# Performance work log

Measured on AMD Instinct MI355X. Metric: run time of the kernel, lower is better.

The kernel has to match this reference:

```python
import jax, jax.numpy as jnp
import numpy as np

EPS = 1e-10
BETA = 1.0  # beta passed to VectorQuantizer in Encoder_conv


def _conv(x, w, b, stride, pad):
    # x: NCHW, w: OIHW
    y = jax.lax.conv_general_dilated(x, w, window_strides=stride, padding=pad,
                                     dimension_numbers=('NCHW', 'OIHW', 'NCHW'))
    if b is not None:
        y = y + b[None, :, None, None]
    return y


def _forward(x, w_in, b_in, w_h1, b_h1, w_h2, b_h2, w_h3, b_h3,
             r0_w1, r0_w2, r1_w1, r1_w2, emb):
    relu = jax.nn.relu
    h = relu(_conv(x, w_in, b_in, (2, 2), [(1, 1), (1, 1)]))      # [B,128,256,256]
    h = relu(_conv(h, w_h1, b_h1, (4, 4), [(2, 2), (2, 2)]))      # [B,256,64,64]
    h = relu(_conv(h, w_h2, b_h2, (4, 4), [(2, 2), (2, 2)]))      # [B,256,16,16]
    h = relu(_conv(h, w_h3, b_h3, (2, 2), [(1, 1), (1, 1)]))      # [B,256,8,8]
    # ResidualBlock with 2 Residual layers: relu->conv[1,3]->relu->conv[1,1], no bias
    for wa, wb in ((r0_w1, r0_w2), (r1_w1, r1_w2)):
        t = _conv(relu(h), wa, None, (1, 1), [(0, 0), (1, 1)])
        t = _conv(relu(t), wb, None, (1, 1), [(0, 0), (0, 0)])
        h = h + t
    h = relu(h)
    # VectorQuantizer
    lat = jnp.transpose(h, (0, 2, 3, 1))                          # [B,H,W,D]
    D = emb.shape[1]
    flat = lat.reshape(-1, D)                                     # [N,D]
    dist = (jnp.sum(flat * flat, axis=1, keepdims=True)
            + jnp.sum(emb * emb, axis=1)
            - 2.0 * flat @ emb.T)                                 # [N,K]
    idx = jnp.argmin(dist, axis=1)                                # [N]
    quant = emb[idx].reshape(lat.shape)                           # [B,H,W,D]
    sg = jax.lax.stop_gradient
    e_loss = jnp.mean((sg(quant) - lat) ** 2)
    q_loss = jnp.mean((quant - sg(lat)) ** 2)
    loss = q_loss + BETA * e_loss
    quant_st = lat + sg(quant - lat)                              # straight-through
    probs = jnp.mean(jax.nn.one_hot(idx, emb.shape[0], dtype=lat.dtype), axis=0)
    perplexity = jnp.exp(-jnp.sum(probs * jnp.log(probs + EPS)))
    return jnp.transpose(quant_st, (0, 3, 1, 2)), loss, perplexity


def setup_inputs() -> dict:
    key = jax.random.key(0)
    ks = jax.random.split(key, 14)
    C_in, C, K = 3, 256, 512
    s = 0.05
    f32 = jnp.float32
    return {
        'x':     jax.random.normal(ks[0], (8, C_in, 512, 512), f32),
        'w_in':  jax.random.normal(ks[1], (C // 2, C_in, 4, 4), f32) * s,
        'b_in':  jnp.zeros((C // 2,), f32),
        'w_h1':  jax.random.normal(ks[2], (C, C // 2, 7, 7), f32) * s,
        'b_h1':  jnp.zeros((C,), f32),
        'w_h2':  jax.random.normal(ks[3], (C, C, 7, 7), f32) * s,
        'b_h2':  jnp.zeros((C,), f32),
        'w_h3':  jax.random.normal(ks[4], (C, C, 3, 3), f32) * s,
        'b_h3':  jnp.zeros((C,), f32),
        'r0_w1': jax.random.normal(ks[5], (4 * C, C, 1, 3), f32) * s,
        'r0_w2': jax.random.normal(ks[6], (C, 4 * C, 1, 1), f32) * s,
        'r1_w1': jax.random.normal(ks[7], (4 * C, C, 1, 3), f32) * s,
        'r1_w2': jax.random.normal(ks[8], (C, 4 * C, 1, 1), f32) * s,
        'emb':   jax.random.uniform(ks[9], (K, C), f32, -1.0 / K, 1.0 / K),
    }


def reference(x, w_in, b_in, w_h1, b_h1, w_h2, b_h2, w_h3, b_h3,
              r0_w1, r0_w2, r1_w1, r1_w2, emb):
    return _forward(x, w_in, b_in, w_h1, b_h1, w_h2, b_h2, w_h3, b_h3,
                    r0_w1, r0_w2, r1_w1, r1_w2, emb)
```

## Files before the change

### kernel.cpp

```cpp
#include <hip/hip_runtime.h>
#include <hip/hip_bf16.h>

typedef __hip_bfloat16 bf16;
typedef __attribute__((ext_vector_type(4))) float f32x4;
typedef __attribute__((ext_vector_type(8))) short short8;

__device__ __forceinline__ float b2f(bf16 v) { return __bfloat162float(v); }
__device__ __forceinline__ ushort f2bu(float v)
{
    bf16 b = __float2bfloat16(v);
    return *(ushort*)&b;
}
__device__ __forceinline__ uint relu2(uint v)
{
    uint r = v;
    if (r & 0x8000u)     r &= 0xFFFF0000u;
    if (r & 0x80000000u) r &= 0x0000FFFFu;
    return r;
}
__device__ __forceinline__ uint packbf2(float a, float b)
{
    uint lo = f2bu(a), hi = f2bu(b);
    return lo | (hi << 16);
}

typedef const __attribute__((address_space(1))) unsigned int* as1_u32;
typedef __attribute__((address_space(3))) unsigned int* as3_u32;
__device__ __forceinline__ void gld16(const void* g, uint* l)
{
    __builtin_amdgcn_global_load_lds((as1_u32)g, (as3_u32)l, 16, 0, 0);
}

__global__ void init_k(const float* __restrict__ w_in, const float* __restrict__ w_h1,
        const float* __restrict__ w_h2, const float* __restrict__ w_h3,
        const float* __restrict__ r0w1, const float* __restrict__ r0w2,
        const float* __restrict__ r1w1, const float* __restrict__ r1w2,
        const float* __restrict__ emb,
        bf16* __restrict__ wp1, bf16* __restrict__ wpack2, bf16* __restrict__ wpack3,
        bf16* __restrict__ wp4, bf16* __restrict__ wpA0, bf16* __restrict__ wpA1,
        bf16* __restrict__ wpB0, bf16* __restrict__ wpB1,
        float* __restrict__ en, float* __restrict__ mse, int* __restrict__ hist,
        float* __restrict__ zpad)
{
    long long i = (long long)blockIdx.x * 256 + threadIdx.x;
    if (i < 8192) {
        int j = i & 7; int co = (i >> 3) & 127; int kb = i >> 10;
        int k = kb * 8 + j;
        wp1[i] = __float2bfloat16(k < 48 ? w_in[co * 48 + k] : 0.f);
        return;
    }
    i -= 8192;
    if (i < 1638400) {
        int cil = i & 7; int co = (i >> 3) & 255; int r = i >> 11;
        int cib8 = r % 16; int tap = r / 16;
        float v = (tap < 49) ? w_h1[(size_t)co * 6272 + (cib8 * 8 + cil) * 49 + tap] : 0.f;
        wpack2[i] = __float2bfloat16(v);
        return;
    }
    i -= 1638400;
    if (i < 3276800) {
        int cil = i & 7; int co = (i >> 3) & 255; int r = i >> 11;
        int cib8 = r % 32; int tap = r / 32;
        float v = (tap < 49) ? w_h2[(size_t)co * 12544 + (cib8 * 8 + cil) * 49 + tap] : 0.f;
        wpack3[i] = __float2bfloat16(v);
        return;
    }
    i -= 3276800;
    if (i < 589824) {
        int cil = i & 7; int co = (i >> 3) & 255; int r = i >> 11;
        int cib8 = r % 32; int tap = r / 32;
        wp4[i] = __float2bfloat16(w_h3[(size_t)co * 2304 + (cib8 * 8 + cil) * 9 + tap]);
        return;
    }
    i -= 589824;
    if (i < 786432) {
        int cil = i & 7; int co = (i >> 3) & 1023; int r = i >> 13;
        int cib8 = r % 32; int tap = r / 32;
        wpA0[i] = __float2bfloat16(r0w1[(size_t)co * 768 + (cib8 * 8 + cil) * 3 + tap]);
        return;
    }
    i -= 786432;
    if (i < 786432) {
        int cil = i & 7; int co = (i >> 3) & 1023; int r = i >> 13;
        int cib8 = r % 32; int tap = r / 32;
        wpA1[i] = __float2bfloat16(r1w1[(size_t)co * 768 + (cib8 * 8 + cil) * 3 + tap]);
        return;
    }
    i -= 786432;
    if (i < 262144) {
        int cil = i & 7; int co = (i >> 3) & 255; int cib8 = (i >> 11) % 128;
        wpB0[i] = __float2bfloat16(r0w2[(size_t)co * 1024 + cib8 * 8 + cil]);
        return;
    }
    i -= 262144;
    if (i < 262144) {
        int cil = i & 7; int co = (i >> 3) & 255; int cib8 = (i >> 11) % 128;
        wpB1[i] = __float2bfloat16(r1w2[(size_t)co * 1024 + cib8 * 8 + cil]);
        return;
    }
    i -= 262144;
    if (i < 512) {
        const float* e = emb + (size_t)i * 256;
        float s = 0.f;
        for (int d = 0; d < 256; ++d) { float v = e[d]; s += v * v; }
        en[i] = s;
        return;
    }
    i -= 512;
    if (i < 577) {
        if (i == 0) mse[0] = 0.f;
        else if (i < 513) hist[i - 1] = 0;
        else zpad[i - 513] = 0.f;
    }
}

__global__ __launch_bounds__(256) void conv1m_k(const float* __restrict__ x,
        const bf16* __restrict__ wp1, const float* __restrict__ bias,
        bf16* __restrict__ h1c)
{
    int bid = blockIdx.x;
    int pxt = bid & 511, img = bid >> 9;
    int tr = pxt >> 4, tc = pxt & 15;
    int oh0 = tr * 8, ow0 = tc * 16;
    const float* xi = x + (size_t)img * 786432;
    bf16* oT = h1c + (size_t)img * 8388608;

    int t = threadIdx.x;
    int wave = t >> 6, lane = t & 63;
    int quad = lane >> 4, l15 = lane & 15;

    __shared__ ushort xs[4 * 640];
    __shared__ ushort ot[128 * 136];

    int ihb = oh0 * 2 - 1, iwb = ow0 * 2 - 1;
    for (int i = t; i < 1836; i += 256) {
        int ci = i / 612; int r1 = i - ci * 612;
        int ihl = r1 / 34, iwl = r1 - ihl * 34;
        int ih = ihb + ihl, iw = iwb + iwl;
        float v = 0.f;
        if ((unsigned)ih < 512u && (unsigned)iw < 512u)
            v = xi[ci * 262144 + ih * 512 + iw];
        xs[ci * 640 + ihl * 35 + iwl] = f2bu(v);
    }
    for (int i = t; i < 640; i += 256) xs[3 * 640 + i] = 0;
    __syncthreads();

    f32x4 zero = {0.f, 0.f, 0.f, 0.f};
    f32x4 acc[8][2];
    #pragma unroll
    for (int m = 0; m < 8; ++m) { acc[m][0] = zero; acc[m][1] = zero; }

    int ci_b = quad >> 1;
    int kh0 = (quad & 1) * 2;
    int iwl0 = 2 * l15;

    #pragma unroll
    for (int ks = 0; ks < 2; ++ks) {
        union { short8 v; uint u[4]; } b[2];
        #pragma unroll
        for (int nt = 0; nt < 2; ++nt) {
            int py = wave * 2 + nt;
            int base = (ks * 2 + ci_b) * 640 + (2 * py + kh0) * 35 + iwl0;
            b[nt].u[0] = *(const uint*)&xs[base];
            b[nt].u[1] = *(const uint*)&xs[base + 2];
            b[nt].u[2] = *(const uint*)&xs[base + 35];
            b[nt].u[3] = *(const uint*)&xs[base + 37];
        }
        const bf16* abase = wp1 + ((size_t)(ks * 4 + quad) * 128 + l15) * 8;
        #pragma unroll
        for (int m = 0; m < 8; ++m) {
            short8 a = *(const short8*)(abase + m * 16 * 8);
            acc[m][0] = __builtin_amdgcn_mfma_f32_16x16x32_bf16(a, b[0].v, acc[m][0], 0, 0, 0);
            acc[m][1] = __builtin_amdgcn_mfma_f32_16x16x32_bf16(a, b[1].v, acc[m][1], 0, 0, 0);
        }
    }

    #pragma unroll
    for (int m = 0; m < 8; ++m) {
        int cobase = m * 16 + quad * 4;
        float b0 = bias[cobase], b1 = bias[cobase + 1];
        float b2 = bias[cobase + 2], b3 = bias[cobase + 3];
        #pragma unroll
        for (int nt = 0; nt < 2; ++nt) {
            int pxl = (wave * 2 + nt) * 16 + l15;
            uint w0 = packbf2(fmaxf(b0 + acc[m][nt][0], 0.f),
                              fmaxf(b1 + acc[m][nt][1], 0.f));
            uint w1 = packbf2(fmaxf(b2 + acc[m][nt][2], 0.f),
                              fmaxf(b3 + acc[m][nt][3], 0.f));
            *(uint*)&ot[pxl * 136 + cobase]     = w0;
            *(uint*)&ot[pxl * 136 + cobase + 2] = w1;
        }
    }
    __syncthreads();
    {
        int pxl = t >> 1, half = t & 1;
        int oh = oh0 + (pxl >> 4), ow = ow0 + (pxl & 15);
        size_t px = (size_t)(oh * 256 + ow);
        #pragma unroll
        for (int cb = 0; cb < 4; ++cb) {
            int c16 = half * 4 + cb;
            const uint4* src = (const uint4*)&ot[pxl * 136 + c16 * 16];
            uint4* dst = (uint4*)(oT + ((size_t)c16 * 65536 + px) * 16);
            dst[0] = src[0];
            dst[1] = src[1];
        }
    }
}

template <int IH, int OH, int CI, int SPLIT, int MODE>
__global__ __launch_bounds__(256, 2) void conv_mfma7_k(
        const bf16* __restrict__ inC, const bf16* __restrict__ wpack,
        const float* __restrict__ bias, float* __restrict__ outA,
        bf16* __restrict__ outT, const float* __restrict__ zpad)
{
    constexpr int TPD = OH / 8;
    constexpr int NT = TPD * TPD;
    constexpr int CPB = (CI / 16) / SPLIT;
    constexpr int CIB8 = CI / 8;
    constexpr int NPX = IH * IH;
    constexpr int SLOTS = 2496;

    int bid = blockIdx.x;
    int pxt = bid % NT;
    int rest = bid / NT;
    int img = rest & 7;
    int split = rest >> 3;
    int oh0 = (pxt / TPD) * 8, ow0 = (pxt % TPD) * 8;

    int t = threadIdx.x;
    int wave = t >> 6, lane = t & 63;
    int quad = lane >> 4, l15 = lane & 15;

    const bf16* inb = inC + (size_t)img * ((size_t)NPX * CI);

    __shared__ __align__(16) uint bufA[SLOTS * 4];
    __shared__ __align__(16) uint bufB[SLOTS * 4];

    f32x4 zero = {0.f, 0.f, 0.f, 0.f};
    f32x4 acc[4][4];
    #pragma unroll
    for (int a = 0; a < 4; ++a)
        #pragma unroll
        for (int b = 0; b < 4; ++b) acc[a][b] = zero;

    int ihb = oh0 * 4 - 2, iwb = ow0 * 4 - 2;
    int qxl = l15 & 7, pyl = l15 >> 3;
    int tap_par = quad >> 1, ci_half = quad & 1;

    int  srel[10];
    bool sval[10];
    #pragma unroll
    for (int it = 0; it < 10; ++it) {
        int sb = (it < 9) ? it * 256 + wave * 64 : 2304 + wave * 64;
        int p  = sb + lane;
        int pb = p << 4;
        int lb = pb ^ (((pb >> 7) & 7) << 4);
        int j  = lb >> 4;
        int pos = j >> 1, half = j & 1;
        int r = pos / 35, c = pos - r * 35;
        int ih = ihb + r, iw = iwb + c;
        sval[it] = (j < 2450) && ((unsigned)ih < (unsigned)IH)
                   && ((unsigned)iw < (unsigned)IH);
        srel[it] = (ih * IH + iw) * 16 + half * 8;
    }

    auto stage = [&](int ch, uint* dst) {
        const bf16* cbp = inb + (size_t)ch * NPX * 16;
        #pragma unroll
        for (int it = 0; it < 10; ++it) {
            if (it == 9 && wave >= 3) continue;
            int sb = (it < 9) ? it * 256 + wave * 64 : 2304 + wave * 64;
            const void* src = sval[it] ? (const void*)(cbp + srel[it])
                                       : (const void*)zpad;
            gld16(src, dst + sb * 4);
        }
    };

    int rbase = pyl * 4480 + qxl * 128 + ci_half * 16;
    int d1  = tap_par * 32;
    int d29 = tap_par * 928;

    auto compute = [&](int ch, const uint* cbuf) {
        const bf16* ab = wpack
            + ((size_t)(ch * 2 + ci_half) * 256 + wave * 64 + l15) * 8
            + (size_t)tap_par * (CIB8 * 2048);
        __builtin_amdgcn_s_setprio(1);
        #pragma unroll
        for (int tp = 0; tp < 25; ++tp) {
            const int kh0 = (2 * tp) / 7, kw0 = (2 * tp) % 7;
            const int cE  = (kh0 * 35 + kw0) * 32;
            int dsel = (tp == 24) ? 0 : ((kw0 == 6) ? d29 : d1);
            int lbb  = rbase + cE + dsel;
            const bf16* at = ab + (size_t)(2 * tp) * (CIB8 * 2048);
            short8 a0 = *(const short8*)(at);
            short8 a1 = *(const short8*)(at + 128);
            short8 a2 = *(const short8*)(at + 256);
            short8 a3 = *(const short8*)(at + 384);
            #pragma unroll
            for (int pt = 0; pt < 4; ++pt) {
                int lb = lbb + pt * 8960;
                int pb = lb ^ (((lb >> 7) & 7) << 4);
                short8 b = *(const short8*)((const char*)cbuf + pb);
                acc[0][pt] = __builtin_amdgcn_mfma_f32_16x16x32_bf16(a0, b, acc[0][pt], 0, 0, 0);
                acc[1][pt] = __builtin_amdgcn_mfma_f32_16x16x32_bf16(a1, b, acc[1][pt], 0, 0, 0);
                acc[2][pt] = __builtin_amdgcn_mfma_f32_16x16x32_bf16(a2, b, acc[2][pt], 0, 0, 0);
                acc[3][pt] = __builtin_amdgcn_mfma_f32_16x16x32_bf16(a3, b, acc[3][pt], 0, 0, 0);
            }
        }
        __builtin_amdgcn_s_setprio(0);
    };

    stage(split * CPB, bufA);
    __syncthreads();
    for (int cc2 = 0; cc2 < CPB; cc2 += 2) {
        stage(split * CPB + cc2 + 1, bufB);
        compute(split * CPB + cc2, bufA);
        __syncthreads();
        if (cc2 + 2 < CPB) stage(split * CPB + cc2 + 2, bufA);
        compute(split * CPB + cc2 + 1, bufB);
        __syncthreads();
    }

    #pragma unroll
    for (int ct = 0; ct < 4; ++ct) {
        int cobase = wave * 64 + ct * 16 + quad * 4;
        #pragma unroll
        for (int pt = 0; pt < 4; ++pt) {
            int px = pt * 16 + l15;
            int oh = oh0 + (px >> 3), ow = ow0 + (px & 7);
            int pxg = oh * OH + ow;
            #pragma unroll
            for (int r = 0; r < 4; ++r) {
                int co = cobase + r;
                float v = acc[ct][pt][r];
                if (MODE == 3) {
                    outA[(size_t)split * ((size_t)8 * OH * OH * 256)
                         + (size_t)img * (OH * OH * 256)
                         + (size_t)co * (OH * OH) + pxg] = v;
                } else {
                    float o = fmaxf(bias[co] + v, 0.f);
                    size_t base = (size_t)img * (size_t)(OH * OH * 256);
                    outT[base + ((size_t)(co >> 4) * (OH * OH) + pxg) * 16 + (co & 15)]
                        = __float2bfloat16(o);
                }
            }
        }
    }
}

__global__ void combine3_k(const float* __restrict__ p3, const float* __restrict__ bias,
                           bf16* __restrict__ h3T)
{
    int idx = blockIdx.x * 256 + threadIdx.x;
    int px = idx & 255;
    int co = (idx >> 8) & 255;
    int img = idx >> 16;
    float v = bias[co];
    #pragma unroll
    for (int s = 0; s < 8; ++s) v += p3[(size_t)s * 524288 + idx];
    v = fmaxf(v, 0.f);
    h3T[((size_t)img * 256 + px) * 256 + co] = __float2bfloat16(v);
}

__global__ __launch_bounds__(256) void conv4m_k(const bf16* __restrict__ h3T,
        const bf16* __restrict__ wp4, const float* __restrict__ bias,
        bf16* __restrict__ h4T)
{
    int bid = blockIdx.x;
    int img = bid >> 2, cog = bid & 3;
    int t = threadIdx.x;
    int wave = t >> 6, lane = t & 63;
    int quad = lane >> 4, l15 = lane & 15;

    __shared__ uint pt[16 * 325];

    for (int i = t; i < 16 * 325; i += 256) pt[i] = 0;

    f32x4 zero = {0.f, 0.f, 0.f, 0.f};
    f32x4 acc[4];
    #pragma unroll
    for (int b = 0; b < 4; ++b) acc[b] = zero;

    const bf16* inb = h3T + (size_t)img * 65536;

    for (int ch = 0; ch < 8; ++ch) {
        __syncthreads();
        for (int e = t; e < 4096; e += 256) {
            int cp = e & 15, px = e >> 4;
            int py = px >> 4, qx = px & 15;
            uint v = *(const uint*)(inb + (size_t)px * 256 + ch * 32 + cp * 2);
            pt[cp * 325 + (py + 1) * 18 + qx + 1] = v;
        }
        __syncthreads();

        for (int tap = 0; tap < 9; ++tap) {
            int kh = tap / 3, kw = tap - kh * 3;
            const bf16* abase = wp4 + ((size_t)((tap * 32 + ch * 4 + quad) * 256)
                                       + cog * 64 + wave * 16 + l15) * 8;
            short8 a = *(const short8*)abase;
            #pragma unroll
            for (int pq = 0; pq < 4; ++pq) {
                int pyo = 2 * pq + (l15 >> 3);
                int ipos = (2 * pyo + kh) * 18 + 2 * (l15 & 7) + kw;
                union { short8 v; uint u[4]; } b;
                b.u[0] = pt[(quad * 4 + 0) * 325 + ipos];
                b.u[1] = pt[(quad * 4 + 1) * 325 + ipos];
                b.u[2] = pt[(quad * 4 + 2) * 325 + ipos];
                b.u[3] = pt[(quad * 4 + 3) * 325 + ipos];
                acc[pq] = __builtin_amdgcn_mfma_f32_16x16x32_bf16(
                    a, b.v, acc[pq], 0, 0, 0);
            }
        }
    }

    int cobase = cog * 64 + wave * 16 + quad * 4;
    #pragma unroll
    for (int pq = 0; pq < 4; ++pq) {
        int px = pq * 16 + l15;
        #pragma unroll
        for (int r = 0; r < 4; ++r) {
            int co = cobase + r;
            float v = fmaxf(bias[co] + acc[pq][r], 0.f);
            h4T[((size_t)img * 64 + px) * 256 + co] = __float2bfloat16(v);
        }
    }
}

__global__ __launch_bounds__(256) void resam_k(const bf16* __restrict__ hT,
        const bf16* __restrict__ wpA, bf16* __restrict__ t1T)
{
    int bid = blockIdx.x;
    int img = bid >> 3, g = bid & 7;
    int t = threadIdx.x;
    int wave = t >> 6, lane = t & 63;
    int quad = lane >> 4, l15 = lane & 15;

    __shared__ uint ph[128 * 81];

    for (int i = t; i < 128 * 81; i += 256) ph[i] = 0;
    __syncthreads();
    const bf16* inb = hT + (size_t)img * 16384;
    for (int e = t; e < 8192; e += 256) {
        int cp = e & 127, px = e >> 7;
        uint v = relu2(*(const uint*)(inb + (size_t)px * 256 + cp * 2));
        ph[cp * 81 + (px >> 3) * 10 + (px & 7) + 1] = v;
    }
    __syncthreads();

    f32x4 zero = {0.f, 0.f, 0.f, 0.f};
    f32x4 acc[2][4];
    #pragma unroll
    for (int a = 0; a < 2; ++a)
        #pragma unroll
        for (int b = 0; b < 4; ++b) acc[a][b] = zero;

    for (int ch = 0; ch < 8; ++ch) {
        for (int tap = 0; tap < 3; ++tap) {
            const bf16* abase = wpA + ((size_t)(tap * 32 + ch * 4 + quad) * 1024
                                       + g * 128 + wave * 32 + l15) * 8;
            short8 a[2];
            #pragma unroll
            for (int ct = 0; ct < 2; ++ct)
                a[ct] = *(const short8*)(abase + ct * 16 * 8);
            #pragma unroll
            for (int pq = 0; pq < 4; ++pq) {
                int py = 2 * pq + (l15 >> 3);
                int pos = py * 10 + (l15 & 7) + tap;
                union { short8 v; uint u[4]; } b;
                b.u[0] = ph[(ch * 16 + quad * 4 + 0) * 81 + pos];
                b.u[1] = ph[(ch * 16 + quad * 4 + 1) * 81 + pos];
                b.u[2] = ph[(ch * 16 + quad * 4 + 2) * 81 + pos];
                b.u[3] = ph[(ch * 16 + quad * 4 + 3) * 81 + pos];
                #pragma unroll
                for (int ct = 0; ct < 2; ++ct)
                    acc[ct][pq] = __builtin_amdgcn_mfma_f32_16x16x32_bf16(
                        a[ct], b.v, acc[ct][pq], 0, 0, 0);
            }
        }
    }

    #pragma unroll
    for (int ct = 0; ct < 2; ++ct) {
        int cobase = g * 128 + wave * 32 + ct * 16 + quad * 4;
        #pragma unroll
        for (int pq = 0; pq < 4; ++pq) {
            int px = pq * 16 + l15;
            #pragma unroll
            for (int r = 0; r < 4; ++r)
                t1T[((size_t)img * 64 + px) * 1024 + cobase + r]
                    = __float2bfloat16(acc[ct][pq][r]);
        }
    }
}

__global__ __launch_bounds__(256) void resbm_k(const bf16* __restrict__ holdT,
        const bf16* __restrict__ t1T, const bf16* __restrict__ wpB,
        bf16* __restrict__ hnewT)
{
    int bid = blockIdx.x;
    int img = bid >> 2, cog = bid & 3;
    int t = threadIdx.x;
    int wave = t >> 6, lane = t & 63;
    int quad = lane >> 4, l15 = lane & 15;

    __shared__ uint pb[256 * 65];

    f32x4 zero = {0.f, 0.f, 0.f, 0.f};
    f32x4 acc[4];
    #pragma unroll
    for (int b = 0; b < 4; ++b) acc[b] = zero;

    const bf16* inb = t1T + (size_t)img * 65536;

    for (int s = 0; s < 2; ++s) {
        __syncthreads();
        for (int e = t; e < 16384; e += 256) {
            int cp = e & 255, px = e >> 8;
            uint v = relu2(*(const uint*)(inb + (size_t)px * 1024 + s * 512 + cp * 2));
            pb[cp * 65 + px] = v;
        }
        __syncthreads();

        for (int chl = 0; chl < 16; ++chl) {
            int ch = s * 16 + chl;
            const bf16* abase = wpB + ((size_t)(ch * 4 + quad) * 256
                                       + cog * 64 + wave * 16 + l15) * 8;
            short8 a = *(const short8*)abase;
            #pragma unroll
            for (int pq = 0; pq < 4; ++pq) {
                int px = pq * 16 + l15;
                union { short8 v; uint u[4]; } b;
                b.u[0] = pb[(chl * 16 + quad * 4 + 0) * 65 + px];
                b.u[1] = pb[(chl * 16 + quad * 4 + 1) * 65 + px];
                b.u[2] = pb[(chl * 16 + quad * 4 + 2) * 65 + px];
                b.u[3] = pb[(chl * 16 + quad * 4 + 3) * 65 + px];
                acc[pq] = __builtin_amdgcn_mfma_f32_16x16x32_bf16(
                    a, b.v, acc[pq], 0, 0, 0);
            }
        }
    }

    int cobase = cog * 64 + wave * 16 + quad * 4;
    #pragma unroll
    for (int pq = 0; pq < 4; ++pq) {
        int px = pq * 16 + l15;
        #pragma unroll
        for (int r = 0; r < 4; ++r) {
            int co = cobase + r;
            size_t o = ((size_t)img * 64 + px) * 256 + co;
            float v = b2f(holdT[o]) + acc[pq][r];
            hnewT[o] = __float2bfloat16(v);
        }
    }
}

__global__ __launch_bounds__(256) void vq_k(const bf16* __restrict__ h6T,
        const float* __restrict__ emb, const float* __restrict__ en,
        float* __restrict__ out, float* __restrict__ mse_acc, int* __restrict__ hist)
{
    int row0 = blockIdx.x * 4;
    int t = threadIdx.x;
    int wave = t >> 6, lane = t & 63;
    __shared__ float lat[4][256];
    __shared__ float swd[4][4];
    __shared__ int   swi[4][4];
    __shared__ int   fidx[4];
    __shared__ float smse[4];

    for (int e = t; e < 1024; e += 256) {
        int r = e >> 8, c = e & 255;
        lat[r][c] = fmaxf(b2f(h6T[(size_t)(row0 + r) * 256 + c]), 0.f);
    }
    __syncthreads();

    float a0[4] = {0.f, 0.f, 0.f, 0.f}, a1[4] = {0.f, 0.f, 0.f, 0.f};
    const float4* e0 = (const float4*)(emb + (size_t)t * 256);
    const float4* e1 = (const float4*)(emb + (size_t)(t + 256) * 256);
    for (int d4 = 0; d4 < 64; ++d4) {
        float4 v0 = e0[d4], v1 = e1[d4];
        #pragma unroll
        for (int r = 0; r < 4; ++r) {
            float l0 = lat[r][d4 * 4], l1 = lat[r][d4 * 4 + 1];
            float l2 = lat[r][d4 * 4 + 2], l3 = lat[r][d4 * 4 + 3];
            a0[r] += l0 * v0.x + l1 * v0.y + l2 * v0.z + l3 * v0.w;
            a1[r] += l0 * v1.x + l1 * v1.y + l2 * v1.z + l3 * v1.w;
        }
    }
    float en0 = en[t], en1 = en[t + 256];
    float bd[4]; int bi[4];
    #pragma unroll
    for (int r = 0; r < 4; ++r) {
        float d0 = en0 - 2.f * a0[r], d1v = en1 - 2.f * a1[r];
        bd[r] = d0; bi[r] = t;
        if (d1v < bd[r]) { bd[r] = d1v; bi[r] = t + 256; }
    }
    #pragma unroll
    for (int s = 1; s < 64; s <<= 1) {
        #pragma unroll
        for (int r = 0; r < 4; ++r) {
            float od = __shfl_xor(bd[r], s);
            int   oi = __shfl_xor(bi[r], s);
            if (od < bd[r] || (od == bd[r] && oi < bi[r])) { bd[r] = od; bi[r] = oi; }
        }
    }
    if (lane == 0) {
        #pragma unroll
        for (int r = 0; r < 4; ++r) { swd[wave][r] = bd[r]; swi[wave][r] = bi[r]; }
    }
    __syncthreads();
    if (t < 4) {
        float best = swd[0][t]; int bidx = swi[0][t];
        for (int w = 1; w < 4; ++w) {
            float od = swd[w][t]; int oi = swi[w][t];
            if (od < best || (od == best && oi < bidx)) { best = od; bidx = oi; }
        }
        fidx[t] = bidx;
    }
    __syncthreads();

    float msel = 0.f;
    #pragma unroll
    for (int r = 0; r < 4; ++r) {
        int row = row0 + r;
        int b = row >> 6, y = (row >> 3) & 7, xx = row & 7;
        float q = emb[(size_t)fidx[r] * 256 + t];
        out[((size_t)(b * 256 + t) * 8 + y) * 8 + xx] = q;
        float diff = q - lat[r][t];
        msel += diff * diff;
    }
    #pragma unroll
    for (int s = 1; s < 64; s <<= 1) msel += __shfl_xor(msel, s);
    if (lane == 0) smse[wave] = msel;
    __syncthreads();
    if (t == 0) atomicAdd(mse_acc, smse[0] + smse[1] + smse[2] + smse[3]);
    if (t < 4) atomicAdd(&hist[fidx[t]], 1);
}

__global__ void final_k(const float* __restrict__ mse_acc, const int* __restrict__ hist,
                        float* __restrict__ out)
{
    __shared__ float sh[512];
    int t = threadIdx.x;
    float p = (float)hist[t] / 512.f;
    sh[t] = p * logf(p + 1e-10f);
    __syncthreads();
    for (int s = 256; s > 0; s >>= 1) {
        if (t < s) sh[t] += sh[t + s];
        __syncthreads();
    }
    if (t == 0) {
        float loss = 2.f * mse_acc[0] / (512.f * 256.f);
        float perp = expf(-sh[0]);
        out[131072] = loss;
        out[131073] = perp;
    }
}

extern "C" void kernel_launch(void* const* d_in, const int* in_sizes, int n_in,
                              void* d_out, int out_size, void* d_ws, size_t ws_size,
                              hipStream_t stream)
{
    const float* x    = (const float*)d_in[0];
    const float* w_in = (const float*)d_in[1];
    const float* b_in = (const float*)d_in[2];
    const float* w_h1 = (const float*)d_in[3];
    const float* b_h1 = (const float*)d_in[4];
    const float* w_h2 = (const float*)d_in[5];
    const float* b_h2 = (const float*)d_in[6];
    const float* w_h3 = (const float*)d_in[7];
    const float* b_h3 = (const float*)d_in[8];
    const float* r0w1 = (const float*)d_in[9];
    const float* r0w2 = (const float*)d_in[10];
    const float* r1w1 = (const float*)d_in[11];
    const float* r1w2 = (const float*)d_in[12];
    const float* emb  = (const float*)d_in[13];
    float* out = (float*)d_out;

    char* ws = (char*)d_ws;
    size_t off = 0;
    auto alloc = [&](size_t bytes) -> void* {
        void* p = ws + off;
        off += (bytes + 255) & ~(size_t)255;
        return p;
    };

    float* en  = (float*)alloc(512 * 4);
    float* mse = (float*)alloc(256);
    int*  hist = (int*)alloc(512 * 4);
    float* zpad = (float*)alloc(256);
    float* p3  = (float*)alloc(4194304ull * 4);
    bf16* h3T  = (bf16*)alloc(524288ull * 2);
    bf16* h4T  = (bf16*)alloc(131072ull * 2);
    bf16* t1T  = (bf16*)alloc(524288ull * 2);
    bf16* h5T  = (bf16*)alloc(131072ull * 2);
    bf16* h6T  = (bf16*)alloc(131072ull * 2);
    bf16* wp1  = (bf16*)alloc(8192ull * 2);
    bf16* wpack2 = (bf16*)alloc(1638400ull * 2);
    bf16* wpack3 = (bf16*)alloc(3276800ull * 2);
    bf16* wp4  = (bf16*)alloc(589824ull * 2);
    bf16* wpA0 = (bf16*)alloc(786432ull * 2);
    bf16* wpA1 = (bf16*)alloc(786432ull * 2);
    bf16* wpB0 = (bf16*)alloc(262144ull * 2);
    bf16* wpB1 = (bf16*)alloc(262144ull * 2);
    bf16* h2c  = (bf16*)alloc(8388608ull * 2);
    size_t base_end = off;

    const size_t H1F_B = 8388608ull * 8 * 2;
    size_t needT1 = base_end + H1F_B + 4096;
    bf16* h1c;
    int tier;
    if (ws_size >= needT1) {
        h1c = (bf16*)alloc(H1F_B);
        tier = 1;
    } else {
        h1c = (bf16*)alloc(8388608ull * 2);
        tier = 2;
    }

    init_k<<<29733, 256, 0, stream>>>(w_in, w_h1, w_h2, w_h3, r0w1, r0w2, r1w1, r1w2,
        emb, wp1, wpack2, wpack3, wp4, wpA0, wpA1, wpB0, wpB1, en, mse, hist, zpad);

    if (tier == 1) {
        conv1m_k<<<4096, 256, 0, stream>>>(x, wp1, b_in, h1c);
        conv_mfma7_k<256, 64, 128, 1, 0><<<512, 256, 0, stream>>>(
            h1c, wpack2, b_h1, nullptr, h2c, zpad);
    } else {
        for (int n = 0; n < 8; ++n) {
            conv1m_k<<<512, 256, 0, stream>>>(x + (size_t)n * 786432, wp1, b_in, h1c);
            conv_mfma7_k<256, 64, 128, 1, 0><<<64, 256, 0, stream>>>(
                h1c, wpack2, b_h1, nullptr, h2c + (size_t)n * 1048576, zpad);
        }
    }

    conv_mfma7_k<64, 16, 256, 8, 3><<<256, 256, 0, stream>>>(
        h2c, wpack3, nullptr, p3, nullptr, zpad);
    combine3_k<<<2048, 256, 0, stream>>>(p3, b_h2, h3T);

    conv4m_k<<<32, 256, 0, stream>>>(h3T, wp4, b_h3, h4T);
    resam_k<<<64, 256, 0, stream>>>(h4T, wpA0, t1T);
    resbm_k<<<32, 256, 0, stream>>>(h4T, t1T, wpB0, h5T);
    resam_k<<<64, 256, 0, stream>>>(h5T, wpA1, t1T);
    resbm_k<<<32, 256, 0, stream>>>(h5T, t1T, wpB1, h6T);

    vq_k<<<128, 256, 0, stream>>>(h6T, emb, en, out, mse, hist);
    final_k<<<1, 512, 0, stream>>>(mse, hist, out);
}
```

Measured before the change: 466.3 us.

## Retile conv waves to 2x2 pixel/channel split and coalesce weight packing

The 7x7 conv kernel now splits its four waves into two pixel halves by two output-channel halves, so each wave runs 8 channel tiles by 2 pixel tiles instead of 4 by 4. This doubles the global weight-fragment loads per LDS activation read and halves LDS reads, moving pressure from LDS to global/L2 weight traffic and raising register use for the A fragments. Separately, the init kernel is rewritten to stage each output channel's weights in LDS and write packed 16-byte vectors. This replaces the previous per-element strided gathers.

```diff
diff --git a/kernel.cpp b/kernel.cpp
--- a/kernel.cpp
+++ b/kernel.cpp
@@ -31,7 +31,8 @@
     __builtin_amdgcn_global_load_lds((as1_u32)g, (as3_u32)l, 16, 0, 0);
 }
 
-__global__ void init_k(const float* __restrict__ w_in, const float* __restrict__ w_h1,
+__global__ __launch_bounds__(256) void initw_k(
+        const float* __restrict__ w_in, const float* __restrict__ w_h1,
         const float* __restrict__ w_h2, const float* __restrict__ w_h3,
         const float* __restrict__ r0w1, const float* __restrict__ r0w2,
         const float* __restrict__ r1w1, const float* __restrict__ r1w2,
@@ -42,76 +43,107 @@
         float* __restrict__ en, float* __restrict__ mse, int* __restrict__ hist,
         float* __restrict__ zpad)
 {
-    long long i = (long long)blockIdx.x * 256 + threadIdx.x;
-    if (i < 8192) {
+    __shared__ ushort ls[12544];
+    int b = blockIdx.x, t = threadIdx.x;
+
+    if (b < 256) {
+        const float* src = w_h1 + (size_t)b * 6272;
+        for (int i = t; i < 6272; i += 256) ls[i] = f2bu(src[i]);
+        __syncthreads();
+        for (int e = t; e < 800; e += 256) {
+            int tap = e >> 4, cib8 = e & 15;
+            short8 v;
+            #pragma unroll
+            for (int cil = 0; cil < 8; ++cil)
+                v[cil] = (tap < 49) ? (short)ls[(cib8 * 8 + cil) * 49 + tap] : (short)0;
+            *(short8*)(wpack2 + ((size_t)(tap * 16 + cib8) * 256 + b) * 8) = v;
+        }
+        return;
+    }
+    if (b < 512) {
+        int co = b - 256;
+        const float* src = w_h2 + (size_t)co * 12544;
+        for (int i = t; i < 12544; i += 256) ls[i] = f2bu(src[i]);
+        __syncthreads();
+        for (int e = t; e < 1600; e += 256) {
+            int tap = e >> 5, cib8 = e & 31;
+            short8 v;
+            #pragma unroll
+            for (int cil = 0; cil < 8; ++cil)
+                v[cil] = (tap < 49) ? (short)ls[(cib8 * 8 + cil) * 49 + tap] : (short)0;
+            *(short8*)(wpack3 + ((size_t)(tap * 32 + cib8) * 256 + co) * 8) = v;
+        }
+        return;
+    }
+    if (b < 768) {
+        int co = b - 512;
+        const float* src = w_h3 + (size_t)co * 2304;
+        for (int i = t; i < 2304; i += 256) ls[i] = f2bu(src[i]);
+        __syncthreads();
+        for (int e = t; e < 288; e += 256) {
+            int tap = e >> 5, cib8 = e & 31;
+            short8 v;
+            #pragma unroll
+            for (int cil = 0; cil < 8; ++cil)
+                v[cil] = (short)ls[(cib8 * 8 + cil) * 9 + tap];
+            *(short8*)(wp4 + ((size_t)(tap * 32 + cib8) * 256 + co) * 8) = v;
+        }
+        return;
+    }
+    if (b < 2816) {
+        int r = b - 768;
+        int which = r >> 10;
+        int co = r & 1023;
+        const float* srcb = which ? r1w1 : r0w1;
+        bf16* dstb = which ? wpA1 : wpA0;
+        const float* src = srcb + (size_t)co * 768;
+        for (int i = t; i < 768; i += 256) ls[i] = f2bu(src[i]);
+        __syncthreads();
+        if (t < 96) {
+            int tap = t >> 5, cib8 = t & 31;
+            short8 v;
+            #pragma unroll
+            for (int cil = 0; cil < 8; ++cil)
+                v[cil] = (short)ls[(cib8 * 8 + cil) * 3 + tap];
+            *(short8*)(dstb + ((size_t)(tap * 32 + cib8) * 1024 + co) * 8) = v;
+        }
+        return;
+    }
+    if (b < 3072) {
+        int r = b - 2816;
+        int which = r >> 7;
+        const float* srcb = which ? r1w2 : r0w2;
+        bf16* dstb = which ? wpB1 : wpB0;
+        int c = (r & 127) * 256 + t;
+        int cib8 = c >> 8, co = c & 255;
+        const float* s = srcb + (size_t)co * 1024 + cib8 * 8;
+        short8 v;
+        #pragma unroll
+        for (int cil = 0; cil < 8; ++cil) v[cil] = (short)f2bu(s[cil]);
+        *(short8*)(dstb + (size_t)c * 8) = v;
+        return;
+    }
+    if (b < 3104) {
+        int i = (b - 3072) * 256 + t;
         int j = i & 7; int co = (i >> 3) & 127; int kb = i >> 10;
         int k = kb * 8 + j;
         wp1[i] = __float2bfloat16(k < 48 ? w_in[co * 48 + k] : 0.f);
         return;
     }
-    i -= 8192;
-    if (i < 1638400) {
-        int cil = i & 7; int co = (i >> 3) & 255; int r = i >> 11;
-        int cib8 = r % 16; int tap = r / 16;
-        float v = (tap < 49) ? w_h1[(size_t)co * 6272 + (cib8 * 8 + cil) * 49 + tap] : 0.f;
-        wpack2[i] = __float2bfloat16(v);
+    if (b < 3106) {
+        int row = (b - 3104) * 256 + t;
+        const float4* e = (const float4*)(emb + (size_t)row * 256);
+        float s = 0.f;
+        for (int d4 = 0; d4 < 64; ++d4) {
+            float4 v = e[d4];
+            s += v.x * v.x + v.y * v.y + v.z * v.z + v.w * v.w;
+        }
+        en[row] = s;
         return;
     }
-    i -= 1638400;
-    if (i < 3276800) {
-        int cil = i & 7; int co = (i >> 3) & 255; int r = i >> 11;
-        int cib8 = r % 32; int tap = r / 32;
-        float v = (tap < 49) ? w_h2[(size_t)co * 12544 + (cib8 * 8 + cil) * 49 + tap] : 0.f;
-        wpack3[i] = __float2bfloat16(v);
-        return;
-    }
-    i -= 3276800;
-    if (i < 589824) {
-        int cil = i & 7; int co = (i >> 3) & 255; int r = i >> 11;
-        int cib8 = r % 32; int tap = r / 32;
-        wp4[i] = __float2bfloat16(w_h3[(size_t)co * 2304 + (cib8 * 8 + cil) * 9 + tap]);
-        return;
-    }
-    i -= 589824;
-    if (i < 786432) {
-        int cil = i & 7; int co = (i >> 3) & 1023; int r = i >> 13;
-        int cib8 = r % 32; int tap = r / 32;
-        wpA0[i] = __float2bfloat16(r0w1[(size_t)co * 768 + (cib8 * 8 + cil) * 3 + tap]);
-        return;
-    }
-    i -= 786432;
-    if (i < 786432) {
-        int cil = i & 7; int co = (i >> 3) & 1023; int r = i >> 13;
-        int cib8 = r % 32; int tap = r / 32;
-        wpA1[i] = __float2bfloat16(r1w1[(size_t)co * 768 + (cib8 * 8 + cil) * 3 + tap]);
-        return;
-    }
-    i -= 786432;
-    if (i < 262144) {
-        int cil = i & 7; int co = (i >> 3) & 255; int cib8 = (i >> 11) % 128;
-        wpB0[i] = __float2bfloat16(r0w2[(size_t)co * 1024 + cib8 * 8 + cil]);
-        return;
-    }
-    i -= 262144;
-    if (i < 262144) {
-        int cil = i & 7; int co = (i >> 3) & 255; int cib8 = (i >> 11) % 128;
-        wpB1[i] = __float2bfloat16(r1w2[(size_t)co * 1024 + cib8 * 8 + cil]);
-        return;
-    }
-    i -= 262144;
-    if (i < 512) {
-        const float* e = emb + (size_t)i * 256;
-        float s = 0.f;
-        for (int d = 0; d < 256; ++d) { float v = e[d]; s += v * v; }
-        en[i] = s;
-        return;
-    }
-    i -= 512;
-    if (i < 577) {
-        if (i == 0) mse[0] = 0.f;
-        else if (i < 513) hist[i - 1] = 0;
-        else zpad[i - 513] = 0.f;
-    }
+    if (t == 0) mse[0] = 0.f;
+    for (int i = t; i < 512; i += 256) hist[i] = 0;
+    if (t < 64) zpad[t] = 0.f;
 }
 
 __global__ __launch_bounds__(256) void conv1m_k(const float* __restrict__ x,
@@ -208,7 +240,7 @@
 }
 
 template <int IH, int OH, int CI, int SPLIT, int MODE>
-__global__ __launch_bounds__(256, 2) void conv_mfma7_k(
+__global__ __launch_bounds__(256, 2) void conv_mfma8_k(
         const bf16* __restrict__ inC, const bf16* __restrict__ wpack,
         const float* __restrict__ bias, float* __restrict__ outA,
         bf16* __restrict__ outT, const float* __restrict__ zpad)
@@ -230,6 +262,7 @@
     int t = threadIdx.x;
     int wave = t >> 6, lane = t & 63;
     int quad = lane >> 4, l15 = lane & 15;
+    int pxh = wave >> 1, coh = wave & 1;
 
     const bf16* inb = inC + (size_t)img * ((size_t)NPX * CI);
 
@@ -237,11 +270,11 @@
     __shared__ __align__(16) uint bufB[SLOTS * 4];
 
     f32x4 zero = {0.f, 0.f, 0.f, 0.f};
-    f32x4 acc[4][4];
-    #pragma unroll
-    for (int a = 0; a < 4; ++a)
-        #pragma unroll
-        for (int b = 0; b < 4; ++b) acc[a][b] = zero;
+    f32x4 acc[8][2];
+    #pragma unroll
+    for (int a = 0; a < 8; ++a) {
+        acc[a][0] = zero; acc[a][1] = zero;
+    }
 
     int ihb = oh0 * 4 - 2, iwb = ow0 * 4 - 2;
     int qxl = l15 & 7, pyl = l15 >> 3;
@@ -276,13 +309,13 @@
         }
     };
 
-    int rbase = pyl * 4480 + qxl * 128 + ci_half * 16;
+    int rbase = pxh * 17920 + pyl * 4480 + qxl * 128 + ci_half * 16;
     int d1  = tap_par * 32;
     int d29 = tap_par * 928;
 
     auto compute = [&](int ch, const uint* cbuf) {
         const bf16* ab = wpack
-            + ((size_t)(ch * 2 + ci_half) * 256 + wave * 64 + l15) * 8
+            + ((size_t)(ch * 2 + ci_half) * 256 + coh * 128 + l15) * 8
             + (size_t)tap_par * (CIB8 * 2048);
         __builtin_amdgcn_s_setprio(1);
         #pragma unroll
@@ -292,19 +325,19 @@
             int dsel = (tp == 24) ? 0 : ((kw0 == 6) ? d29 : d1);
             int lbb  = rbase + cE + dsel;
             const bf16* at = ab + (size_t)(2 * tp) * (CIB8 * 2048);
-            short8 a0 = *(const short8*)(at);
-            short8 a1 = *(const short8*)(at + 128);
-            short8 a2 = *(const short8*)(at + 256);
-            short8 a3 = *(const short8*)(at + 384);
-            #pragma unroll
-            for (int pt = 0; pt < 4; ++pt) {
+            short8 a[8];
+            #pragma unroll
+            for (int ct = 0; ct < 8; ++ct)
+                a[ct] = *(const short8*)(at + ct * 128);
+            #pragma unroll
+            for (int pt = 0; pt < 2; ++pt) {
                 int lb = lbb + pt * 8960;
                 int pb = lb ^ (((lb >> 7) & 7) << 4);
                 short8 b = *(const short8*)((const char*)cbuf + pb);
-                acc[0][pt] = __builtin_amdgcn_mfma_f32_16x16x32_bf16(a0, b, acc[0][pt], 0, 0, 0);
-                acc[1][pt] = __builtin_amdgcn_mfma_f32_16x16x32_bf16(a1, b, acc[1][pt], 0, 0, 0);
-                acc[2][pt] = __builtin_amdgcn_mfma_f32_16x16x32_bf16(a2, b, acc[2][pt], 0, 0, 0);
-                acc[3][pt] = __builtin_amdgcn_mfma_f32_16x16x32_bf16(a3, b, acc[3][pt], 0, 0, 0);
+                #pragma unroll
+                for (int ct = 0; ct < 8; ++ct)
+                    acc[ct][pt] = __builtin_amdgcn_mfma_f32_16x16x32_bf16(
+                        a[ct], b, acc[ct][pt], 0, 0, 0);
             }
         }
         __builtin_amdgcn_s_setprio(0);
@@ -322,11 +355,11 @@
     }
 
     #pragma unroll
-    for (int ct = 0; ct < 4; ++ct) {
-        int cobase = wave * 64 + ct * 16 + quad * 4;
-        #pragma unroll
-        for (int pt = 0; pt < 4; ++pt) {
-            int px = pt * 16 + l15;
+    for (int ct = 0; ct < 8; ++ct) {
+        int cobase = coh * 128 + ct * 16 + quad * 4;
+        #pragma unroll
+        for (int pt = 0; pt < 2; ++pt) {
+            int px = pxh * 32 + pt * 16 + l15;
             int oh = oh0 + (px >> 3), ow = ow0 + (px & 7);
             int pxg = oh * OH + ow;
             #pragma unroll
@@ -717,22 +750,22 @@
         tier = 2;
     }
 
-    init_k<<<29733, 256, 0, stream>>>(w_in, w_h1, w_h2, w_h3, r0w1, r0w2, r1w1, r1w2,
+    initw_k<<<3107, 256, 0, stream>>>(w_in, w_h1, w_h2, w_h3, r0w1, r0w2, r1w1, r1w2,
         emb, wp1, wpack2, wpack3, wp4, wpA0, wpA1, wpB0, wpB1, en, mse, hist, zpad);
 
     if (tier == 1) {
         conv1m_k<<<4096, 256, 0, stream>>>(x, wp1, b_in, h1c);
-        conv_mfma7_k<256, 64, 128, 1, 0><<<512, 256, 0, stream>>>(
+        conv_mfma8_k<256, 64, 128, 1, 0><<<512, 256, 0, stream>>>(
             h1c, wpack2, b_h1, nullptr, h2c, zpad);
     } else {
         for (int n = 0; n < 8; ++n) {
             conv1m_k<<<512, 256, 0, stream>>>(x + (size_t)n * 786432, wp1, b_in, h1c);
-            conv_mfma7_k<256, 64, 128, 1, 0><<<64, 256, 0, stream>>>(
+            conv_mfma8_k<256, 64, 128, 1, 0><<<64, 256, 0, stream>>>(
                 h1c, wpack2, b_h1, nullptr, h2c + (size_t)n * 1048576, zpad);
         }
     }
 
-    conv_mfma7_k<64, 16, 256, 8, 3><<<256, 256, 0, stream>>>(
+    conv_mfma8_k<64, 16, 256, 8, 3><<<256, 256, 0, stream>>>(
         h2c, wpack3, nullptr, p3, nullptr, zpad);
     combine3_k<<<2048, 256, 0, stream>>>(p3, b_h2, h3T);
 
```

Measured after the change: 471.5 us. About the same (+1.1%).
